# Kernel tuning notes

Measured on AMD Instinct MI355X. Metric: run time of the kernel, lower is better.

The kernel has to match this reference:

```python
import jax, jax.numpy as jnp
import numpy as np

B, D_IN, H1, H2, OUT = 8, 1024, 2048, 1024, 5120

def setup_inputs() -> dict:
    key = jax.random.key(0)
    ks = jax.random.split(key, 5)
    s1 = (6.0 / (D_IN + H1)) ** 0.5  # xavier_uniform-like scale
    s2 = (6.0 / (H1 + H2)) ** 0.5
    s3 = (6.0 / (H2 + OUT)) ** 0.5
    return {
        "x": jax.random.normal(ks[0], (B, D_IN), dtype=jnp.float32),
        "W1": jax.random.uniform(ks[1], (D_IN, H1), jnp.float32, -s1, s1),
        "b1": jnp.zeros((H1,), jnp.float32),
        "W2": jax.random.uniform(ks[2], (H1, H2), jnp.float32, -s2, s2),
        "b2": jnp.zeros((H2,), jnp.float32),
        "W3": jax.random.uniform(ks[3], (H2, OUT), jnp.float32, -s3, s3),
        "b3": jnp.zeros((OUT,), jnp.float32),
        "CM": jax.random.uniform(ks[4], (OUT, OUT), jnp.float32),
    }

def reference(x, W1, b1, W2, b2, W3, b3, CM):
    # MLP stack (eval mode: dropout is identity)
    h = jax.nn.relu(x @ W1 + b1)
    h = jax.nn.relu(h @ W2 + b2)
    features = h
    logits = h @ W3 + b3                      # [B, OUT]
    # tropical-style correlation: max_k logits[b,k] * CM[o,k]
    out = jnp.max(logits[:, None, :] * CM[None, :, :], axis=-1)  # [B, OUT]
    return out.astype(jnp.float32), features
```

## Files before the change

### kernel.cpp

```cpp
#include <hip/hip_runtime.h>
#include <cstdint>

#define B8   8
#define DIN  1024
#define NH1  2048
#define NH2  1024
#define NOUT 5120

__device__ __forceinline__ float4 ld4(const float* p) {
  return *reinterpret_cast<const float4*>(p);
}
__device__ __forceinline__ void st4(float* p, float4 v) {
  *reinterpret_cast<float4*>(p) = v;
}

template<int K, int N, int KSPLIT, int NPART, bool RELU_IN, bool WRITE_STAGE>
__global__ __launch_bounds__(256)
void gemm8(const float* __restrict__ Asrc, const float* __restrict__ bias_in,
           const float* __restrict__ W, float* __restrict__ Cparts,
           float* __restrict__ stage_out)
{
  constexpr int KC    = K / KSPLIT;
  constexpr int KC4   = KC / 4;
  constexpr int NCOLB = N / 64;
  constexpr int KT    = KC / 16;

  __shared__ float A_lds[8][KC];
  __shared__ float red[16][8][64];

  const int tid = threadIdx.x;
  const int kb  = blockIdx.x / NCOLB;
  const int cb  = blockIdx.x % NCOLB;
  const int k0  = kb * KC;

  for (int e = tid; e < 8 * KC4; e += 256) {
    const int b = e / KC4, k4 = e - b * KC4;
    float4 v;
    if constexpr (NPART == 0) {
      v = ld4(&Asrc[(size_t)b * K + k0 + 4 * k4]);
    } else {
      v = ld4(&bias_in[k0 + 4 * k4]);
      #pragma unroll
      for (int p = 0; p < NPART; ++p) {
        float4 t = ld4(&Asrc[((size_t)p * 8 + b) * K + k0 + 4 * k4]);
        v.x += t.x; v.y += t.y; v.z += t.z; v.w += t.w;
      }
      if constexpr (RELU_IN) {
        v.x = fmaxf(v.x, 0.f); v.y = fmaxf(v.y, 0.f);
        v.z = fmaxf(v.z, 0.f); v.w = fmaxf(v.w, 0.f);
      }
    }
    st4(&A_lds[b][4 * k4], v);
    if constexpr (WRITE_STAGE) {
      if (cb == 0) st4(&stage_out[(size_t)b * K + k0 + 4 * k4], v);
    }
  }
  __syncthreads();

  const int g  = tid & 15, ks = tid >> 4;
  const int c0 = cb * 64 + g * 4;
  float4 acc[8];
  #pragma unroll
  for (int b = 0; b < 8; ++b) acc[b] = make_float4(0.f, 0.f, 0.f, 0.f);

  const float* Wp = &W[(size_t)(k0 + ks * KT) * N + c0];
  #pragma unroll
  for (int i = 0; i < KT; i += 4) {
    const float4 w0 = ld4(Wp + (size_t)(i + 0) * N);
    const float4 w1 = ld4(Wp + (size_t)(i + 1) * N);
    const float4 w2 = ld4(Wp + (size_t)(i + 2) * N);
    const float4 w3 = ld4(Wp + (size_t)(i + 3) * N);
    const int kk = ks * KT + i;
    #pragma unroll
    for (int b = 0; b < 8; ++b) {
      const float4 a = ld4(&A_lds[b][kk]);
      acc[b].x += a.x * w0.x + a.y * w1.x + a.z * w2.x + a.w * w3.x;
      acc[b].y += a.x * w0.y + a.y * w1.y + a.z * w2.y + a.w * w3.y;
      acc[b].z += a.x * w0.z + a.y * w1.z + a.z * w2.z + a.w * w3.z;
      acc[b].w += a.x * w0.w + a.y * w1.w + a.z * w2.w + a.w * w3.w;
    }
  }

  __syncthreads();
  #pragma unroll
  for (int b = 0; b < 8; ++b) st4(&red[ks][b][g * 4], acc[b]);
  __syncthreads();

  for (int p = tid; p < 512; p += 256) {
    const int c = p & 63, b = p >> 6;
    float s = 0.f;
    #pragma unroll
    for (int j = 0; j < 16; ++j) s += red[j][b][c];
    Cparts[((size_t)kb * 8 + b) * N + cb * 64 + c] = s;
  }
}

__global__ __launch_bounds__(256)
void finalize_logits(const float* __restrict__ parts, const float* __restrict__ b3,
                     float* __restrict__ logits)
{
  const int i  = blockIdx.x * 256 + threadIdx.x;
  const int b  = i / 1280, k4 = i - b * 1280;
  float4 v = ld4(&b3[4 * k4]);
  #pragma unroll
  for (int p = 0; p < 4; ++p) {
    const float4 t = ld4(&parts[((size_t)p * 8 + b) * NOUT + 4 * k4]);
    v.x += t.x; v.y += t.y; v.z += t.z; v.w += t.w;
  }
  st4(&logits[(size_t)b * NOUT + 4 * k4], v);
}

__global__ __launch_bounds__(256)
void tropical2r(const float* __restrict__ logits, const float* __restrict__ CM,
                float* __restrict__ out)
{
  const int tid = threadIdx.x;
  const int w   = tid >> 6;
  const int l   = tid & 63;
  const int o0  = (blockIdx.x * 4 + w) * 2;

  const float* cm0 = &CM[(size_t)(o0 + 0) * NOUT + 4 * l];
  const float* cm1 = &CM[(size_t)(o0 + 1) * NOUT + 4 * l];
  const float* lg  = &logits[4 * l];

  float pmax0[8], pmax1[8];
  #pragma unroll
  for (int b = 0; b < 8; ++b) { pmax0[b] = -3.402823466e38f; pmax1[b] = -3.402823466e38f; }

  for (int j = 0; j < 20; ++j) {
    const int off = 256 * j;
    const float4 c0 = ld4(cm0 + off);
    const float4 c1 = ld4(cm1 + off);
    #pragma unroll
    for (int b = 0; b < 8; ++b) {
      const float4 lv = ld4(lg + (size_t)b * NOUT + off);
      const float a0 = fmaxf(lv.x * c0.x, lv.y * c0.y);
      const float a1 = fmaxf(lv.z * c0.z, lv.w * c0.w);
      pmax0[b] = fmaxf(pmax0[b], fmaxf(a0, a1));
      const float b0 = fmaxf(lv.x * c1.x, lv.y * c1.y);
      const float b1 = fmaxf(lv.z * c1.z, lv.w * c1.w);
      pmax1[b] = fmaxf(pmax1[b], fmaxf(b0, b1));
    }
  }

  #pragma unroll
  for (int b = 0; b < 8; ++b) {
    float v0 = pmax0[b], v1 = pmax1[b];
    for (int m = 32; m; m >>= 1) {
      v0 = fmaxf(v0, __shfl_xor(v0, m));
      v1 = fmaxf(v1, __shfl_xor(v1, m));
    }
    if (l == 0) {
      out[(size_t)b * NOUT + o0 + 0] = v0;
      out[(size_t)b * NOUT + o0 + 1] = v1;
    }
  }
}

extern "C" void kernel_launch(void* const* d_in, const int* in_sizes, int n_in,
                              void* d_out, int out_size, void* d_ws, size_t ws_size,
                              hipStream_t stream)
{
  const float* x  = (const float*)d_in[0];
  const float* W1 = (const float*)d_in[1];
  const float* b1 = (const float*)d_in[2];
  const float* W2 = (const float*)d_in[3];
  const float* b2 = (const float*)d_in[4];
  const float* W3 = (const float*)d_in[5];
  const float* b3 = (const float*)d_in[6];
  const float* CM = (const float*)d_in[7];

  float* out  = (float*)d_out;
  float* feat = out + B8 * NOUT;

  float* ws      = (float*)d_ws;
  float* parts1  = ws;
  float* parts2  = parts1 + 8  * 8 * NH1;
  float* parts3  = parts2 + 16 * 8 * NH2;
  float* logits  = parts3 + 4  * 8 * NOUT;

  gemm8<DIN, NH1, 8, 0, false, false><<<256, 256, 0, stream>>>(x, nullptr, W1, parts1, nullptr);
  gemm8<NH1, NH2, 16, 8, true, false><<<256, 256, 0, stream>>>(parts1, b1, W2, parts2, nullptr);
  gemm8<NH2, NOUT, 4, 16, true, true><<<320, 256, 0, stream>>>(parts2, b2, W3, parts3, feat);
  finalize_logits<<<40, 256, 0, stream>>>(parts3, b3, logits);
  tropical2r<<<640, 256, 0, stream>>>(logits, CM, out);
}
```

Baseline: 48.90 us.

## Split tropical max-product over K and compute four output rows per wave

The tropical max-product kernel now splits the 5120-long reduction into five 1024-wide chunks across a second grid dimension. Each wave handles four output rows instead of two, so every logits load is reused across more CM rows. Partial maxima go to workspace and a new combine kernel reduces them. This trades an extra launch and a small partial buffer for more blocks in flight and better reuse of logits loads.

```diff
diff --git a/kernel.cpp b/kernel.cpp
--- a/kernel.cpp
+++ b/kernel.cpp
@@ -6,6 +6,7 @@
 #define NH1  2048
 #define NH2  1024
 #define NOUT 5120
+#define TKS  5
 
 __device__ __forceinline__ float4 ld4(const float* p) {
   return *reinterpret_cast<const float4*>(p);
@@ -110,51 +111,83 @@
   st4(&logits[(size_t)b * NOUT + 4 * k4], v);
 }
 
-__global__ __launch_bounds__(256)
-void tropical2r(const float* __restrict__ logits, const float* __restrict__ CM,
-                float* __restrict__ out)
+__global__ __launch_bounds__(256, 4)
+void tropical4w(const float* __restrict__ logits, const float* __restrict__ CM,
+                float* __restrict__ tpart)
 {
   const int tid = threadIdx.x;
   const int w   = tid >> 6;
   const int l   = tid & 63;
-  const int o0  = (blockIdx.x * 4 + w) * 2;
-
-  const float* cm0 = &CM[(size_t)(o0 + 0) * NOUT + 4 * l];
-  const float* cm1 = &CM[(size_t)(o0 + 1) * NOUT + 4 * l];
-  const float* lg  = &logits[4 * l];
-
-  float pmax0[8], pmax1[8];
-  #pragma unroll
-  for (int b = 0; b < 8; ++b) { pmax0[b] = -3.402823466e38f; pmax1[b] = -3.402823466e38f; }
-
-  for (int j = 0; j < 20; ++j) {
+  const int ks  = blockIdx.y;
+  const int k0  = ks * 1024;
+  const int o0  = (blockIdx.x * 4 + w) * 4;
+
+  const float* cmb = &CM[(size_t)o0 * NOUT + k0 + 4 * l];
+  const float* lg  = &logits[k0 + 4 * l];
+
+  float pm0[8], pm1[8], pm2[8], pm3[8];
+  #pragma unroll
+  for (int b = 0; b < 8; ++b) {
+    pm0[b] = -3.402823466e38f; pm1[b] = -3.402823466e38f;
+    pm2[b] = -3.402823466e38f; pm3[b] = -3.402823466e38f;
+  }
+
+  for (int j = 0; j < 4; ++j) {
     const int off = 256 * j;
-    const float4 c0 = ld4(cm0 + off);
-    const float4 c1 = ld4(cm1 + off);
+    const float4 c0 = ld4(cmb + off);
+    const float4 c1 = ld4(cmb + (size_t)1 * NOUT + off);
+    const float4 c2 = ld4(cmb + (size_t)2 * NOUT + off);
+    const float4 c3 = ld4(cmb + (size_t)3 * NOUT + off);
     #pragma unroll
     for (int b = 0; b < 8; ++b) {
       const float4 lv = ld4(lg + (size_t)b * NOUT + off);
-      const float a0 = fmaxf(lv.x * c0.x, lv.y * c0.y);
-      const float a1 = fmaxf(lv.z * c0.z, lv.w * c0.w);
-      pmax0[b] = fmaxf(pmax0[b], fmaxf(a0, a1));
-      const float b0 = fmaxf(lv.x * c1.x, lv.y * c1.y);
-      const float b1 = fmaxf(lv.z * c1.z, lv.w * c1.w);
-      pmax1[b] = fmaxf(pmax1[b], fmaxf(b0, b1));
-    }
-  }
-
+      float t0, t1;
+      t0 = fmaxf(lv.x * c0.x, lv.y * c0.y);
+      t1 = fmaxf(lv.z * c0.z, lv.w * c0.w);
+      pm0[b] = fmaxf(pm0[b], fmaxf(t0, t1));
+      t0 = fmaxf(lv.x * c1.x, lv.y * c1.y);
+      t1 = fmaxf(lv.z * c1.z, lv.w * c1.w);
+      pm1[b] = fmaxf(pm1[b], fmaxf(t0, t1));
+      t0 = fmaxf(lv.x * c2.x, lv.y * c2.y);
+      t1 = fmaxf(lv.z * c2.z, lv.w * c2.w);
+      pm2[b] = fmaxf(pm2[b], fmaxf(t0, t1));
+      t0 = fmaxf(lv.x * c3.x, lv.y * c3.y);
+      t1 = fmaxf(lv.z * c3.z, lv.w * c3.w);
+      pm3[b] = fmaxf(pm3[b], fmaxf(t0, t1));
+    }
+  }
+
+  float* tp = &tpart[(size_t)ks * 8 * NOUT];
   #pragma unroll
   for (int b = 0; b < 8; ++b) {
-    float v0 = pmax0[b], v1 = pmax1[b];
+    float v0 = pm0[b], v1 = pm1[b], v2 = pm2[b], v3 = pm3[b];
     for (int m = 32; m; m >>= 1) {
       v0 = fmaxf(v0, __shfl_xor(v0, m));
       v1 = fmaxf(v1, __shfl_xor(v1, m));
+      v2 = fmaxf(v2, __shfl_xor(v2, m));
+      v3 = fmaxf(v3, __shfl_xor(v3, m));
     }
     if (l == 0) {
-      out[(size_t)b * NOUT + o0 + 0] = v0;
-      out[(size_t)b * NOUT + o0 + 1] = v1;
-    }
-  }
+      tp[(size_t)b * NOUT + o0 + 0] = v0;
+      tp[(size_t)b * NOUT + o0 + 1] = v1;
+      tp[(size_t)b * NOUT + o0 + 2] = v2;
+      tp[(size_t)b * NOUT + o0 + 3] = v3;
+    }
+  }
+}
+
+__global__ __launch_bounds__(256)
+void tropical_combine(const float* __restrict__ tpart, float* __restrict__ out)
+{
+  const int i = blockIdx.x * 256 + threadIdx.x;
+  float4 v = ld4(&tpart[4 * (size_t)i]);
+  #pragma unroll
+  for (int p = 1; p < TKS; ++p) {
+    const float4 t = ld4(&tpart[(size_t)p * 8 * NOUT + 4 * (size_t)i]);
+    v.x = fmaxf(v.x, t.x); v.y = fmaxf(v.y, t.y);
+    v.z = fmaxf(v.z, t.z); v.w = fmaxf(v.w, t.w);
+  }
+  st4(&out[4 * (size_t)i], v);
 }
 
 extern "C" void kernel_launch(void* const* d_in, const int* in_sizes, int n_in,
@@ -178,10 +211,15 @@
   float* parts2  = parts1 + 8  * 8 * NH1;
   float* parts3  = parts2 + 16 * 8 * NH2;
   float* logits  = parts3 + 4  * 8 * NOUT;
+  float* tpart   = logits + 8 * NOUT;
 
   gemm8<DIN, NH1, 8, 0, false, false><<<256, 256, 0, stream>>>(x, nullptr, W1, parts1, nullptr);
   gemm8<NH1, NH2, 16, 8, true, false><<<256, 256, 0, stream>>>(parts1, b1, W2, parts2, nullptr);
   gemm8<NH2, NOUT, 4, 16, true, true><<<320, 256, 0, stream>>>(parts2, b2, W3, parts3, feat);
   finalize_logits<<<40, 256, 0, stream>>>(parts3, b3, logits);
-  tropical2r<<<640, 256, 0, stream>>>(logits, CM, out);
-}
+  {
+    dim3 grid(320, TKS);
+    tropical4w<<<grid, 256, 0, stream>>>(logits, CM, tpart);
+  }
+  tropical_combine<<<40, 256, 0, stream>>>(tpart, out);
+}
```

New measurement: 59.79 us. 22.3% more time.
